# Performance work log

Hardware: AMD Instinct MI355X
Metric: run time of the kernel (lower is better)

Reference implementation:

```python
import jax, jax.numpy as jnp
import numpy as np

B, S, DIN, DIM = 4, 4096, 256, 256
GAMMA = 0.9865


def setup_inputs() -> dict:
    key = jax.random.key(0)
    ks = jax.random.split(key, 9)
    inp = {
        'xq': jax.random.normal(ks[0], (B, S, DIN), dtype=jnp.float32),
        'xk': jax.random.normal(ks[1], (B, S, DIN), dtype=jnp.float32),
        'xv': jax.random.normal(ks[2], (B, S, DIN), dtype=jnp.float32),
        'Wq': jax.random.normal(ks[3], (DIN, DIM), dtype=jnp.float32) * 0.05,
        'bq': jnp.zeros((DIM,), dtype=jnp.float32),
        'Wk': jax.random.normal(ks[4], (DIN, DIM), dtype=jnp.float32) * 0.05,
        'bk': jnp.zeros((DIM,), dtype=jnp.float32),
        'Wv': jax.random.normal(ks[5], (DIN, DIM), dtype=jnp.float32) * 0.05,
        'bv': jnp.zeros((DIM,), dtype=jnp.float32),
    }
    return inp


def _decay_matrix(s, gamma):
    # D[i, j] = gamma^(i-j) if i >= j else 0
    idx = jnp.arange(s)
    diff = idx[:, None] - idx[None, :]
    D = jnp.where(diff >= 0,
                  jnp.power(jnp.float32(gamma), diff.astype(jnp.float32)),
                  jnp.float32(0.0))
    return D


def reference(xq, xk, xv, Wq, bq, Wk, bk, Wv, bv):
    Q = xq @ Wq + bq  # [B,S,D]
    K = xk @ Wk + bk  # [B,S,D]
    V = xv @ Wv + bv  # [B,S,D]
    d = Q.shape[-1]
    # scores[b,i,j] = Q[b,i] . K[b,j] / sqrt(d)
    x = jnp.einsum('bid,bjd->bij', Q, K) / jnp.sqrt(jnp.float32(d))
    D = _decay_matrix(S, GAMMA)
    # Faithful to TF broadcasting: divides along the LAST axis (per-column by
    # sqrt of that index's row-sum): D[i,j] /= sqrt(sum_k D[j,k])
    D = D / jnp.sqrt(jnp.sum(D, axis=-1))
    x = x * D  # broadcast [B,S,S] * [S,S]
    # _norm_3 per batch element with TF broadcasting: x[b,i,j] /= max(|sum_k x[b,j,k]|, 1)
    denom = jnp.maximum(jnp.abs(jnp.sum(x, axis=-1)), 1.0)  # [B,S]
    x = x / denom[:, None, :]
    return x @ V  # [B,S,D]
```

## Files before the change

### kernel.cpp

```cpp
#include <hip/hip_runtime.h>
#include <math.h>

#define BB 4
#define SS 4096
#define DD 256
#define LL 256
#define NCH 16
#define GAMMA 0.9865f
#define LOG2G (-0.019609034f)
#define INV1MG 74.07407407f
#define SLAB 1032
#define SLABB 520

typedef __attribute__((ext_vector_type(8))) short short8;
typedef __attribute__((ext_vector_type(4))) float f32x4;
typedef unsigned short u16;
typedef unsigned int u32;

__device__ __forceinline__ u16 f2bf(float f) {
  union { float f; unsigned u; } v; v.f = f;
  unsigned r = v.u + 0x7FFFu + ((v.u >> 16) & 1u);
  return (u16)(r >> 16);
}
__device__ __forceinline__ float bf2f(u16 h) {
  union { unsigned u; float f; } v; v.u = ((unsigned)h) << 16; return v.f;
}

__device__ __forceinline__ void gll16(const u16* g, u16* l) {
  __builtin_amdgcn_global_load_lds(
      (const __attribute__((address_space(1))) u32*)g,
      (__attribute__((address_space(3))) u32*)l, 16, 0, 0);
}
__device__ __forceinline__ void stage8kp(const u16* g, u16* l, int lane) {
#pragma unroll
  for (int i = 0; i < 8; ++i)
    gll16(g + i * 512 + lane * 8, l + (i >> 1) * SLAB + (i & 1) * 512);
}

__device__ __forceinline__ void mfma_step_regB64(
    const u16* Ah, const u16* Al, const short8 bh[4], const short8 bl[4],
    int fm, int fq, f32x4 acc[4][4])
{
  const int ka = fq * SLABB;
  short8 ah[4], al[4];
#pragma unroll
  for (int i = 0; i < 4; ++i) {
    ah[i] = *(const short8*)&Ah[ka + (i * 16 + fm) * 8];
    al[i] = *(const short8*)&Al[ka + (i * 16 + fm) * 8];
  }
#pragma unroll
  for (int j = 0; j < 4; ++j)
#pragma unroll
    for (int i = 0; i < 4; ++i) {
      acc[i][j] = __builtin_amdgcn_mfma_f32_16x16x32_bf16(al[i], bh[j], acc[i][j], 0, 0, 0);
      acc[i][j] = __builtin_amdgcn_mfma_f32_16x16x32_bf16(ah[i], bl[j], acc[i][j], 0, 0, 0);
      acc[i][j] = __builtin_amdgcn_mfma_f32_16x16x32_bf16(ah[i], bh[j], acc[i][j], 0, 0, 0);
    }
}

__device__ __forceinline__ void mfma_step_regB_ab(
    const u16* Ah, const u16* Al, const short8 bh[2], const short8 bl[2],
    int wm0, int fm, int fq, f32x4 acc[4][2])
{
  const int ka = fq * SLAB;
  short8 ah[4], al[4];
#pragma unroll
  for (int i = 0; i < 4; ++i) {
    ah[i] = *(const short8*)&Ah[ka + (wm0 + i * 16 + fm) * 8];
    al[i] = *(const short8*)&Al[ka + (wm0 + i * 16 + fm) * 8];
  }
#pragma unroll
  for (int j = 0; j < 2; ++j)
#pragma unroll
    for (int i = 0; i < 4; ++i) {
      acc[i][j] = __builtin_amdgcn_mfma_f32_16x16x32_bf16(al[i], bh[j], acc[i][j], 0, 0, 0);
      acc[i][j] = __builtin_amdgcn_mfma_f32_16x16x32_bf16(ah[i], bl[j], acc[i][j], 0, 0, 0);
      acc[i][j] = __builtin_amdgcn_mfma_f32_16x16x32_bf16(ah[i], bh[j], acc[i][j], 0, 0, 0);
    }
}

__device__ __forceinline__ void loadB2(short8 bh[2], short8 bl[2],
    const u16* BhP, const u16* BlP, int ks, int wn0, int fm, int fq)
{
  const int base = ks * 4096 + fq * 1024;
#pragma unroll
  for (int j = 0; j < 2; ++j) {
    int o = base + (wn0 + j * 16 + fm) * 8;
    bh[j] = *(const short8*)&BhP[o];
    bl[j] = *(const short8*)&BlP[o];
  }
}

__device__ __forceinline__ void mfma_step_ab(
    const u16* Ah, const u16* Al, const u16* Bh, const u16* Bl,
    int wm0, int wn0, int fm, int fq, f32x4 acc[4][2])
{
  const int ka = fq * SLAB, kb = fq * SLABB;
  short8 ah[4], al[4];
#pragma unroll
  for (int i = 0; i < 4; ++i) {
    ah[i] = *(const short8*)&Ah[ka + (wm0 + i * 16 + fm) * 8];
    al[i] = *(const short8*)&Al[ka + (wm0 + i * 16 + fm) * 8];
  }
#pragma unroll
  for (int j = 0; j < 2; ++j) {
    short8 bh = *(const short8*)&Bh[kb + (wn0 + j * 16 + fm) * 8];
    short8 bl = *(const short8*)&Bl[kb + (wn0 + j * 16 + fm) * 8];
#pragma unroll
    for (int i = 0; i < 4; ++i) {
      acc[i][j] = __builtin_amdgcn_mfma_f32_16x16x32_bf16(al[i], bh, acc[i][j], 0, 0, 0);
      acc[i][j] = __builtin_amdgcn_mfma_f32_16x16x32_bf16(ah[i], bl, acc[i][j], 0, 0, 0);
      acc[i][j] = __builtin_amdgcn_mfma_f32_16x16x32_bf16(ah[i], bh, acc[i][j], 0, 0, 0);
    }
  }
}

__global__ __launch_bounds__(256) void init_pack_kernel(
    const float* __restrict__ Wq, const float* __restrict__ Wk, const float* __restrict__ Wv,
    u16* __restrict__ Wth, u16* __restrict__ Wtl,
    float* __restrict__ rsP, float* __restrict__ lVec)
{
  const int which = blockIdx.x;
  const int it = blockIdx.y;
  const int t = threadIdx.x;
  if (which == 0) {
    *(float4*)&rsP[(size_t)(it * 256 + t) * 4] = (float4){0.f, 0.f, 0.f, 0.f};
  } else if (which == 1) {
    *(float4*)&lVec[(size_t)(it * 256 + t) * 4] = (float4){0.f, 0.f, 0.f, 0.f};
  }
  const float* W = which == 0 ? Wq : (which == 1 ? Wk : Wv);
  for (int pn = 0; pn < 2; ++pn) {
    int pos = it * 256 + t;
    int k8 = pos >> 7, r = pos & 127;
    u16 hs[8], ls[8];
#pragma unroll
    for (int u = 0; u < 8; ++u) {
      float x = W[(size_t)(k8 * 8 + u) * DD + pn * 128 + r];
      u16 h = f2bf(x); hs[u] = h; ls[u] = f2bf(x - bf2f(h));
    }
    size_t o = ((size_t)((which * 2 + pn) * 32 + k8)) * 1024 + (size_t)r * 8;
    *(short8*)&Wth[o] = *(short8*)hs;
    *(short8*)&Wtl[o] = *(short8*)ls;
  }
}

__global__ __launch_bounds__(256, 3) void proj_kernel(
    const float* __restrict__ xq, const float* __restrict__ xk, const float* __restrict__ xv,
    const u16* __restrict__ Wth, const u16* __restrict__ Wtl,
    const float* __restrict__ bq, const float* __restrict__ bk_, const float* __restrict__ bv,
    u16* __restrict__ Qh, u16* __restrict__ Ql,
    u16* __restrict__ Kh, u16* __restrict__ Kl,
    u16* __restrict__ KTh, u16* __restrict__ KTl,
    u16* __restrict__ VTh, u16* __restrict__ VTl,
    float* __restrict__ lVec)
{
  const int which = blockIdx.z;
  const float* bias = which == 0 ? bq : (which == 1 ? bk_ : bv);
  const int m0 = blockIdx.x * 64;
  __shared__ u16 SM[16 * SLABB];
  __shared__ float rsc[64];
  __shared__ float wlut[64];
  __shared__ float kacc[64];
  float* fb = (float*)SM;
  const int tid = threadIdx.x, lane = tid & 63, wave = tid >> 6;
  const int wn0g = wave * 64;
  const int fm = lane & 15, fq = lane >> 4;
  if (which == 1 && tid < 64) {
    int sb = (m0 & (SS - 1)) + tid;
    rsc[tid] = rsqrtf((1.0f - exp2f((float)(sb + 1) * LOG2G)) * INV1MG);
    wlut[tid] = exp2f((float)(255 - ((m0 & (LL - 1)) + tid)) * LOG2G);
    kacc[tid] = 0.f;
  }
  const float* XP = (which == 0 ? xq : (which == 1 ? xk : xv)) + (size_t)m0 * DD;
  const int pnw = wn0g >> 7, wl = wn0g & 127;
  const u16* WhP = Wth + (size_t)((which * 2 + pnw) * 32) * 1024;
  const u16* WlP = Wtl + (size_t)((which * 2 + pnw) * 32) * 1024;
  const int arow = tid >> 2, ak8 = tid & 3;
  f32x4 acc[4][4];
#pragma unroll
  for (int i = 0; i < 4; ++i)
#pragma unroll
    for (int j = 0; j < 4; ++j) acc[i][j] = (f32x4){0.f, 0.f, 0.f, 0.f};
  float xs[8];
  short8 bh[4], bl[4];
  {
    const int base = fq * 1024;
#pragma unroll
    for (int j = 0; j < 4; ++j) {
      int o = base + (wl + j * 16 + fm) * 8;
      bh[j] = *(const short8*)&WhP[o];
      bl[j] = *(const short8*)&WlP[o];
    }
  }
  {
    const float* src = XP + (size_t)arow * DD + ak8 * 8;
    *(float4*)&xs[0] = *(const float4*)src;
    *(float4*)&xs[4] = *(const float4*)(src + 4);
    u16 hs[8], ls[8];
#pragma unroll
    for (int u = 0; u < 8; ++u) {
      u16 h = f2bf(xs[u]); hs[u] = h; ls[u] = f2bf(xs[u] - bf2f(h));
    }
    *(short8*)&SM[ak8 * SLABB + arow * 8] = *(short8*)hs;
    *(short8*)&SM[4 * SLABB + ak8 * SLABB + arow * 8] = *(short8*)ls;
  }
  int cur = 0;
  for (int ks = 0; ks < 8; ++ks) {
    __syncthreads();
    u16* Ac = SM + cur * 8 * SLABB;
    u16* An = SM + (cur ^ 1) * 8 * SLABB;
    if (ks < 7) {
      const float* src = XP + (size_t)arow * DD + (ks + 1) * 32 + ak8 * 8;
      *(float4*)&xs[0] = *(const float4*)src;
      *(float4*)&xs[4] = *(const float4*)(src + 4);
    }
    mfma_step_regB64(Ac, Ac + 4 * SLABB, bh, bl, fm, fq, acc);
    if (ks < 7) {
      const int base = (ks + 1) * 4096 + fq * 1024;
#pragma unroll
      for (int j = 0; j < 4; ++j) {
        int o = base + (wl + j * 16 + fm) * 8;
        bh[j] = *(const short8*)&WhP[o];
        bl[j] = *(const short8*)&WlP[o];
      }
      u16 hs[8], ls[8];
#pragma unroll
      for (int u = 0; u < 8; ++u) {
        u16 h = f2bf(xs[u]); hs[u] = h; ls[u] = f2bf(xs[u] - bf2f(h));
      }
      *(short8*)&An[ak8 * SLABB + arow * 8] = *(short8*)hs;
      *(short8*)&An[4 * SLABB + ak8 * SLABB + arow * 8] = *(short8*)ls;
    }
    cur ^= 1;
  }
  const int b = m0 >> 12, sbb = m0 & (SS - 1);
  for (int p = 0; p < 4; ++p) {
    __syncthreads();
    if (wn0g == p * 64) {
#pragma unroll
      for (int i = 0; i < 4; ++i)
#pragma unroll
        for (int j = 0; j < 4; ++j)
#pragma unroll
          for (int r = 0; r < 4; ++r)
            fb[(i * 16 + fq * 4 + r) * 65 + j * 16 + fm] = acc[i][j][r];
    }
    __syncthreads();
    if (which == 0) {
#pragma unroll
      for (int it = 0; it < 2; ++it) {
        int unit = it * 256 + tid;
        int k8l = unit >> 6, row = unit & 63;
        int gc0 = p * 64 + k8l * 8;
        u16 hs[8], ls[8];
#pragma unroll
        for (int u = 0; u < 8; ++u) {
          float v = (fb[row * 65 + k8l * 8 + u] + bias[gc0 + u]) * (1.f / 16.f);
          u16 h = f2bf(v); hs[u] = h; ls[u] = f2bf(v - bf2f(h));
        }
        size_t o = (size_t)(m0 >> 7) * 32768 + (size_t)(p * 8 + k8l) * 1024 +
                   (size_t)((m0 & 64) + row) * 8;
        *(short8*)&Qh[o] = *(short8*)hs;
        *(short8*)&Ql[o] = *(short8*)ls;
      }
    } else if (which == 1) {
#pragma unroll
      for (int it = 0; it < 2; ++it) {
        int unit = it * 256 + tid;
        int k8l = unit >> 6, row = unit & 63;
        int gc0 = p * 64 + k8l * 8;
        u16 hs[8], ls[8];
#pragma unroll
        for (int u = 0; u < 8; ++u) {
          float v = (fb[row * 65 + k8l * 8 + u] + bias[gc0 + u]) * rsc[row];
          u16 h = f2bf(v); hs[u] = h; ls[u] = f2bf(v - bf2f(h));
        }
        size_t o = (size_t)(m0 >> 7) * 32768 + (size_t)(p * 8 + k8l) * 1024 +
                   (size_t)((m0 & 64) + row) * 8;
        *(short8*)&Kh[o] = *(short8*)hs;
        *(short8*)&Kl[o] = *(short8*)ls;
      }
      float kpart = 0.f;
#pragma unroll
      for (int it = 0; it < 2; ++it) {
        int unit = it * 256 + tid;
        int dl = unit & 63, s8l = unit >> 6;
        int gcolg = p * 64 + dl;
        float bs = bias[gcolg];
        u16 hs[8], ls[8];
#pragma unroll
        for (int u = 0; u < 8; ++u) {
          int row = s8l * 8 + u;
          float v = (fb[row * 65 + dl] + bs) * rsc[row];
          kpart = fmaf(v, wlut[row], kpart);
          u16 h = f2bf(v); hs[u] = h; ls[u] = f2bf(v - bf2f(h));
        }
        int sb0 = sbb + s8l * 8;
        size_t o = ((size_t)(b * 2 + (gcolg >> 7)) * 512 + (sb0 >> 3)) * 1024 + (size_t)(gcolg & 127) * 8;
        *(short8*)&KTh[o] = *(short8*)hs;
        *(short8*)&KTl[o] = *(short8*)ls;
      }
      atomicAdd(&kacc[tid & 63], kpart);
      __syncthreads();
      if (tid < 64) {
        int c = sbb >> 8;
        atomicAdd(&lVec[(size_t)(b * NCH + c) * DD + p * 64 + tid], kacc[tid]);
        kacc[tid] = 0.f;
      }
    } else {
#pragma unroll
      for (int it = 0; it < 2; ++it) {
        int unit = it * 256 + tid;
        int dl = unit & 63, s8l = unit >> 6;
        int gcolg = p * 64 + dl;
        float bs = bias[gcolg];
        u16 hs[8], ls[8];
#pragma unroll
        for (int u = 0; u < 8; ++u) {
          float v = fb[(s8l * 8 + u) * 65 + dl] + bs;
          u16 h = f2bf(v); hs[u] = h; ls[u] = f2bf(v - bf2f(h));
        }
        int sb0 = sbb + s8l * 8;
        size_t o = ((size_t)(b * 2 + (gcolg >> 7)) * 512 + (sb0 >> 3)) * 1024 + (size_t)(gcolg & 127) * 8;
        *(short8*)&VTh[o] = *(short8*)hs;
        *(short8*)&VTl[o] = *(short8*)ls;
      }
    }
  }
}

__global__ __launch_bounds__(256, 4) void scores_kernel(
    const u16* __restrict__ Qh, const u16* __restrict__ Ql,
    const u16* __restrict__ Kh, const u16* __restrict__ Kl,
    const float* __restrict__ lVec, u16* __restrict__ Sgh, u16* __restrict__ Sgl,
    float* __restrict__ rsP)
{
  const int chunk = blockIdx.x, b = chunk >> 4, c = chunk & 15;
  const int y = blockIdx.y;
  const int m0 = (y < 2) ? 0 : 128;
  const int jn0 = (y < 2) ? y * 64 : (y - 2) * 64;
  __shared__ u16 SA[2 * 8 * SLAB];
  __shared__ float cv[256], lut[256], rowAcc[128], qd2[2][128];
  float* fb = (float*)SA;
  const int tid = threadIdx.x, lane = tid & 63, wave = tid >> 6;
  const int wm0 = (wave >> 1) * 64, wn0 = (wave & 1) * 32;
  const int fm = lane & 15, fq = lane >> 4;
  if (jn0 == 0) {
    const float gL = exp2f((float)LL * LOG2G);
    float s = 0.f;
    for (int cp = 0; cp < c; ++cp)
      s = fmaf(gL, s, lVec[(size_t)(b * NCH + cp) * DD + tid]);
    cv[tid] = s;
  }
  lut[tid] = exp2f((float)tid * LOG2G);
  if (tid < 128) rowAcc[tid] = 0.f;
  const int growA = b * SS + c * LL + m0;
  const int growB = b * SS + c * LL + jn0;
  const u16* QhP = Qh + (size_t)(growA >> 7) * 32768;
  const u16* QlP = Ql + (size_t)(growA >> 7) * 32768;
  const u16* KhP = Kh + (size_t)(growB >> 7) * 32768 + (size_t)(growB & 127) * 8;
  const u16* KlP = Kl + (size_t)(growB >> 7) * 32768 + (size_t)(growB & 127) * 8;
  f32x4 acc[4][2];
#pragma unroll
  for (int i = 0; i < 4; ++i)
#pragma unroll
    for (int j = 0; j < 2; ++j) acc[i][j] = (f32x4){0.f, 0.f, 0.f, 0.f};
  float qdreg = 0.f;
  const int qrow = tid & 127, qk8b = tid >> 7;
  short8 bh[2], bl[2];
  if (wave == 0) stage8kp(QhP, SA, lane);
  if (wave == 1) stage8kp(QlP, SA + 4 * SLAB, lane);
  loadB2(bh, bl, KhP, KlP, 0, wn0, fm, fq);
  int cur = 0;
  for (int ks = 0; ks < 8; ++ks) {
    __syncthreads();
    u16* Ac = cur ? SA + 8 * SLAB : SA;
    u16* An = cur ? SA : SA + 8 * SLAB;
    if (ks < 7) {
      if (wave == 0) stage8kp(QhP + (ks + 1) * 4096, An, lane);
      if (wave == 1) stage8kp(QlP + (ks + 1) * 4096, An + 4 * SLAB, lane);
    }
    mfma_step_regB_ab(Ac, Ac + 4 * SLAB, bh, bl, wm0, fm, fq, acc);
    if (ks < 7) loadB2(bh, bl, KhP, KlP, ks + 1, wn0, fm, fq);
    if (jn0 == 0) {
#pragma unroll
      for (int h2 = 0; h2 < 2; ++h2) {
        int k8l = qk8b + 2 * h2;
        const u16* ahp = &Ac[k8l * SLAB + qrow * 8];
        const u16* alp = &Ac[4 * SLAB + k8l * SLAB + qrow * 8];
#pragma unroll
        for (int u = 0; u < 8; ++u)
          qdreg = fmaf(bf2f(ahp[u]) + bf2f(alp[u]), cv[ks * 32 + k8l * 8 + u], qdreg);
      }
    }
    cur ^= 1;
  }
  qd2[qk8b][qrow] = qdreg;
  const int ps = chunk * 2 + (m0 >> 7);
  for (int rh = 0; rh < 2; ++rh) {
    __syncthreads();
    if (wm0 == rh * 64) {
#pragma unroll
      for (int i = 0; i < 4; ++i)
#pragma unroll
        for (int j = 0; j < 2; ++j)
#pragma unroll
          for (int r = 0; r < 4; ++r)
            fb[(i * 16 + fq * 4 + r) * 65 + wn0 + j * 16 + fm] = acc[i][j][r];
    }
    __syncthreads();
#pragma unroll
    for (int it = 0; it < 2; ++it) {
      int unit = it * 256 + tid;
      int k8l = unit >> 6, rowl = unit & 63;
      int il = m0 + rh * 64 + rowl;
      int jlb = jn0 + k8l * 8;
      float part = 0.f;
      u16 hs[8], ls[8];
#pragma unroll
      for (int u = 0; u < 8; ++u) {
        int jl = jlb + u;
        float v = (jl <= il) ? fb[rowl * 65 + k8l * 8 + u] * lut[il - jl] : 0.f;
        part += v;
        u16 h = f2bf(v); hs[u] = h; ls[u] = f2bf(v - bf2f(h));
      }
      atomicAdd(&rowAcc[rh * 64 + rowl], part);
      size_t o = (size_t)(ps * 32 + (jn0 >> 3) + k8l) * 1024 + (size_t)(rh * 64 + rowl) * 8;
      *(short8*)&Sgh[o] = *(short8*)hs;
      *(short8*)&Sgl[o] = *(short8*)ls;
    }
  }
  __syncthreads();
  if (tid < 128) {
    float rs = rowAcc[tid];
    if (jn0 == 0)
      rs += exp2f((float)(m0 + tid + 1) * LOG2G) * (qd2[0][tid] + qd2[1][tid]);
    atomicAdd(&rsP[(size_t)b * SS + c * LL + m0 + tid], rs);
  }
}

__global__ __launch_bounds__(256, 4) void lmat_kernel(
    const u16* __restrict__ VTh, const u16* __restrict__ VTl,
    const float* __restrict__ rsP,
    const u16* __restrict__ KTh, const u16* __restrict__ KTl,
    float* __restrict__ lMatT)
{
  const int chunk = blockIdx.x, b = chunk >> 4, c = chunk & 15;
  const int ty = blockIdx.y;
  const int m0 = (ty >> 2) * 128, n0 = (ty & 3) * 64;
  __shared__ u16 SA[2 * 8 * SLAB];
  __shared__ float swl[256];
  const int tid = threadIdx.x, lane = tid & 63, wave = tid >> 6;
  const int wm0 = (wave >> 1) * 64, wn0 = (wave & 1) * 32;
  const int fm = lane & 15, fq = lane >> 4;
  swl[tid] = exp2f((float)(255 - tid) * LOG2G) /
             fmaxf(fabsf(rsP[(size_t)b * SS + c * LL + tid]), 1.0f);
  const u16* AThP = VTh + ((size_t)(b * 2 + (m0 >> 7)) * 512 + c * 32) * 1024;
  const u16* ATlP = VTl + ((size_t)(b * 2 + (m0 >> 7)) * 512 + c * 32) * 1024;
  const u16* BhP = KTh + ((size_t)(b * 2 + (n0 >> 7)) * 512 + c * 32) * 1024 + (size_t)(n0 & 127) * 8;
  const u16* BlP = KTl + ((size_t)(b * 2 + (n0 >> 7)) * 512 + c * 32) * 1024 + (size_t)(n0 & 127) * 8;
  const int arow = tid >> 1;
  f32x4 acc[4][2];
#pragma unroll
  for (int i = 0; i < 4; ++i)
#pragma unroll
    for (int j = 0; j < 2; ++j) acc[i][j] = (f32x4){0.f, 0.f, 0.f, 0.f};
  short8 vh[2], vl[2];
  short8 bh[2], bl[2];
  loadB2(bh, bl, BhP, BlP, 0, wn0, fm, fq);
#pragma unroll
  for (int t = 0; t < 2; ++t) {
    int ak8 = (tid & 1) * 2 + t;
    int off = ak8 * 1024 + arow * 8;
    vh[t] = *(const short8*)&AThP[off];
    vl[t] = *(const short8*)&ATlP[off];
  }
  __syncthreads();
#pragma unroll
  for (int t = 0; t < 2; ++t) {
    int ak8 = (tid & 1) * 2 + t;
    u16 hs[8], ls[8];
#pragma unroll
    for (int u = 0; u < 8; ++u) {
      float v = (bf2f((u16)vh[t][u]) + bf2f((u16)vl[t][u])) * swl[ak8 * 8 + u];
      u16 h = f2bf(v); hs[u] = h; ls[u] = f2bf(v - bf2f(h));
    }
    *(short8*)&SA[ak8 * SLAB + arow * 8] = *(short8*)hs;
    *(short8*)&SA[4 * SLAB + ak8 * SLAB + arow * 8] = *(short8*)ls;
  }
  int cur = 0;
  for (int ks = 0; ks < 8; ++ks) {
    __syncthreads();
    u16* Ac = cur ? SA + 8 * SLAB : SA;
    u16* An = cur ? SA : SA + 8 * SLAB;
    if (ks < 7) {
#pragma unroll
      for (int t = 0; t < 2; ++t) {
        int ak8 = (tid & 1) * 2 + t;
        int off = ((ks + 1) * 4 + ak8) * 1024 + arow * 8;
        vh[t] = *(const short8*)&AThP[off];
        vl[t] = *(const short8*)&ATlP[off];
      }
    }
    mfma_step_regB_ab(Ac, Ac + 4 * SLAB, bh, bl, wm0, fm, fq, acc);
    if (ks < 7) {
      loadB2(bh, bl, BhP, BlP, ks + 1, wn0, fm, fq);
#pragma unroll
      for (int t = 0; t < 2; ++t) {
        int ak8 = (tid & 1) * 2 + t;
        u16 hs[8], ls[8];
#pragma unroll
        for (int u = 0; u < 8; ++u) {
          float v = (bf2f((u16)vh[t][u]) + bf2f((u16)vl[t][u])) *
                    swl[(ks + 1) * 32 + ak8 * 8 + u];
          u16 h = f2bf(v); hs[u] = h; ls[u] = f2bf(v - bf2f(h));
        }
        *(short8*)&An[ak8 * SLAB + arow * 8] = *(short8*)hs;
        *(short8*)&An[4 * SLAB + ak8 * SLAB + arow * 8] = *(short8*)ls;
      }
    }
    cur ^= 1;
  }
#pragma unroll
  for (int i = 0; i < 4; ++i)
#pragma unroll
    for (int j = 0; j < 2; ++j)
#pragma unroll
      for (int r = 0; r < 4; ++r) {
        int e = m0 + wm0 + i * 16 + fq * 4 + r;
        int d = n0 + wn0 + j * 16 + fm;
        lMatT[(size_t)chunk * 65536 + (size_t)e * 256 + d] = acc[i][j][r];
      }
}

__global__ __launch_bounds__(256) void combine_mat_kernel(
    const float* __restrict__ lMatT, u16* __restrict__ cMh, u16* __restrict__ cMl)
{
  const int t = blockIdx.x * 256 + threadIdx.x;
  const int b = t >> 13, rem = t & 8191;
  const int k8 = rem >> 8, e = rem & 255;
  const float gL = powf(GAMMA, (float)LL);
  float s[8] = {0.f, 0.f, 0.f, 0.f, 0.f, 0.f, 0.f, 0.f};
  for (int ch = 0; ch < 16; ++ch) {
    size_t ro = (size_t)(b * 16 + ch) * 65536 + (size_t)e * 256 + k8 * 8;
    float4 a0 = *(const float4*)&lMatT[ro];
    float4 a1 = *(const float4*)&lMatT[ro + 4];
    float vals[8] = {a0.x, a0.y, a0.z, a0.w, a1.x, a1.y, a1.z, a1.w};
    u16 hh[8], ll[8];
#pragma unroll
    for (int u = 0; u < 8; ++u) {
      u16 h = f2bf(s[u]); hh[u] = h; ll[u] = f2bf(s[u] - bf2f(h));
    }
    size_t wo = ((size_t)(((b * 16 + ch) * 2 + (e >> 7)) * 32 + k8)) * 1024 + (size_t)(e & 127) * 8;
    *(short8*)&cMh[wo] = *(short8*)hh;
    *(short8*)&cMl[wo] = *(short8*)ll;
#pragma unroll
    for (int u = 0; u < 8; ++u) s[u] = gL * s[u] + vals[u];
  }
}

__global__ __launch_bounds__(256, 3) void out_kernel(
    const u16* __restrict__ Qh, const u16* __restrict__ Ql,
    const u16* __restrict__ cMh, const u16* __restrict__ cMl,
    const u16* __restrict__ Sgh, const u16* __restrict__ Sgl,
    const u16* __restrict__ VTh, const u16* __restrict__ VTl,
    const float* __restrict__ rsP,
    float* __restrict__ out)
{
  const int chunk = blockIdx.x, b = chunk >> 4, c = chunk & 15;
  const int ty = blockIdx.y;
  const int m0 = (ty >> 2) * 128, n0 = (ty & 3) * 64;
  __shared__ u16 SA[2 * 8 * SLAB];
  __shared__ u16 SB[2 * 8 * SLABB];
  __shared__ float olut[128];
  __shared__ float sdn[256];
  const int tid = threadIdx.x, lane = tid & 63, wave = tid >> 6;
  const int wm0 = (wave >> 1) * 64, wn0 = (wave & 1) * 32;
  const int fm = lane & 15, fq = lane >> 4;
  if (tid < 128) olut[tid] = exp2f((float)(m0 + tid + 1) * LOG2G);
  sdn[tid] = 1.0f / fmaxf(fabsf(rsP[(size_t)b * SS + c * LL + tid]), 1.0f);
  f32x4 acc[4][2];
#pragma unroll
  for (int i = 0; i < 4; ++i)
#pragma unroll
    for (int j = 0; j < 2; ++j) acc[i][j] = (f32x4){0.f, 0.f, 0.f, 0.f};
  int cur = 0;
  {
    const u16* AhP = Qh + (size_t)(b * 32 + c * 2 + (m0 >> 7)) * 32768;
    const u16* AlP = Ql + (size_t)(b * 32 + c * 2 + (m0 >> 7)) * 32768;
    const u16* BhP = cMh + (size_t)(chunk * 2 + (n0 >> 7)) * 32768 + (size_t)(n0 & 127) * 8;
    const u16* BlP = cMl + (size_t)(chunk * 2 + (n0 >> 7)) * 32768 + (size_t)(n0 & 127) * 8;
    short8 bh[2], bl[2];
    if (wave == 0) stage8kp(AhP, SA, lane);
    if (wave == 1) stage8kp(AlP, SA + 4 * SLAB, lane);
    loadB2(bh, bl, BhP, BlP, 0, wn0, fm, fq);
    for (int ks = 0; ks < 8; ++ks) {
      __syncthreads();
      u16* Ac = cur ? SA + 8 * SLAB : SA;
      u16* An = cur ? SA : SA + 8 * SLAB;
      if (ks < 7) {
        if (wave == 0) stage8kp(AhP + (ks + 1) * 4096, An, lane);
        if (wave == 1) stage8kp(AlP + (ks + 1) * 4096, An + 4 * SLAB, lane);
      }
      mfma_step_regB_ab(Ac, Ac + 4 * SLAB, bh, bl, wm0, fm, fq, acc);
      if (ks < 7) loadB2(bh, bl, BhP, BlP, ks + 1, wn0, fm, fq);
      cur ^= 1;
    }
  }
  {
    const u16* AhP = Sgh + (size_t)(chunk * 2 + (m0 >> 7)) * 32768;
    const u16* AlP = Sgl + (size_t)(chunk * 2 + (m0 >> 7)) * 32768;
    const u16* BThP = VTh + ((size_t)(b * 2 + (n0 >> 7)) * 512 + c * 32) * 1024 + (size_t)(n0 & 127) * 8;
    const u16* BTlP = VTl + ((size_t)(b * 2 + (n0 >> 7)) * 512 + c * 32) * 1024 + (size_t)(n0 & 127) * 8;
    const int ber = tid >> 2, bk8 = tid & 3;
    const int nks = (m0 >> 5) + 4;
    short8 vh, vl;
    {
      u16* Ac = cur ? SA + 8 * SLAB : SA;
      u16* Bc = cur ? SB + 8 * SLABB : SB;
      if (wave == 0) stage8kp(AhP, Ac, lane);
      if (wave == 1) stage8kp(AlP, Ac + 4 * SLAB, lane);
      int off = bk8 * 1024 + ber * 8;
      vh = *(const short8*)&BThP[off];
      vl = *(const short8*)&BTlP[off];
#pragma unroll
      for (int i = 0; i < 4; ++i)
#pragma unroll
        for (int r = 0; r < 4; ++r) {
          int rl = wm0 + i * 16 + fq * 4 + r;
          float sc = olut[rl];
#pragma unroll
          for (int j = 0; j < 2; ++j) acc[i][j][r] *= sc;
        }
      u16 hs[8], ls[8];
#pragma unroll
      for (int u = 0; u < 8; ++u) {
        float v = (bf2f((u16)vh[u]) + bf2f((u16)vl[u])) * sdn[bk8 * 8 + u];
        u16 h = f2bf(v); hs[u] = h; ls[u] = f2bf(v - bf2f(h));
      }
      *(short8*)&Bc[bk8 * SLABB + ber * 8] = *(short8*)hs;
      *(short8*)&Bc[4 * SLABB + bk8 * SLABB + ber * 8] = *(short8*)ls;
    }
    for (int ks = 0; ks < nks; ++ks) {
      __syncthreads();
      u16* Ac = cur ? SA + 8 * SLAB : SA;
      u16* Bc = cur ? SB + 8 * SLABB : SB;
      u16* An = cur ? SA : SA + 8 * SLAB;
      u16* Bn = cur ? SB : SB + 8 * SLABB;
      if (ks + 1 < nks) {
        if (wave == 0) stage8kp(AhP + (ks + 1) * 4096, An, lane);
        if (wave == 1) stage8kp(AlP + (ks + 1) * 4096, An + 4 * SLAB, lane);
        int off = ((ks + 1) * 4 + bk8) * 1024 + ber * 8;
        vh = *(const short8*)&BThP[off];
        vl = *(const short8*)&BTlP[off];
      }
      mfma_step_ab(Ac, Ac + 4 * SLAB, Bc, Bc + 4 * SLABB, wm0, wn0, fm, fq, acc);
      if (ks + 1 < nks) {
        u16 hs[8], ls[8];
#pragma unroll
        for (int u = 0; u < 8; ++u) {
          float v = (bf2f((u16)vh[u]) + bf2f((u16)vl[u])) *
                    sdn[(ks + 1) * 32 + bk8 * 8 + u];
          u16 h = f2bf(v); hs[u] = h; ls[u] = f2bf(v - bf2f(h));
        }
        *(short8*)&Bn[bk8 * SLABB + ber * 8] = *(short8*)hs;
        *(short8*)&Bn[4 * SLABB + bk8 * SLABB + ber * 8] = *(short8*)ls;
      }
      cur ^= 1;
    }
  }
#pragma unroll
  for (int i = 0; i < 4; ++i)
#pragma unroll
    for (int j = 0; j < 2; ++j)
#pragma unroll
      for (int r = 0; r < 4; ++r) {
        int il = m0 + wm0 + i * 16 + fq * 4 + r;
        int e = n0 + wn0 + j * 16 + fm;
        out[(size_t)(b * SS + c * LL + il) * DD + e] = acc[i][j][r];
      }
}

extern "C" void kernel_launch(void* const* d_in, const int* in_sizes, int n_in,
                              void* d_out, int out_size, void* d_ws, size_t ws_size,
                              hipStream_t stream) {
  const float* xq = (const float*)d_in[0];
  const float* xk = (const float*)d_in[1];
  const float* xv = (const float*)d_in[2];
  const float* Wq = (const float*)d_in[3];
  const float* bq = (const float*)d_in[4];
  const float* Wk = (const float*)d_in[5];
  const float* bk = (const float*)d_in[6];
  const float* Wv = (const float*)d_in[7];
  const float* bv = (const float*)d_in[8];
  float* out = (float*)d_out;

  char* p = (char*)d_ws;
  const size_t H16 = (size_t)BB * SS * DD * 2;
  u16* Qh   = (u16*)(p + 0 * H16);  u16* Ql   = (u16*)(p + 1 * H16);
  u16* Kh   = (u16*)(p + 2 * H16);  u16* Kl   = (u16*)(p + 3 * H16);
  u16* KTh  = (u16*)(p + 4 * H16);  u16* KTl  = (u16*)(p + 5 * H16);
  u16* VTh  = (u16*)(p + 6 * H16);  u16* VTl  = (u16*)(p + 7 * H16);
  u16* Sgh  = (u16*)(p + 10 * H16); u16* Sgl  = (u16*)(p + 11 * H16);
  u16* cMh  = (u16*)(p + 12 * H16); u16* cMl  = (u16*)(p + 13 * H16);
  float* lMatT = (float*)(p + 14 * H16);
  u16* Wth = (u16*)(p + 18 * H16);
  u16* Wtl = (u16*)(p + 18 * H16 + 3 * DD * DD * 2);
  float* rsP  = (float*)(p + 18 * H16 + 6 * DD * DD * 2);
  float* lVec = rsP + (size_t)BB * SS;

  init_pack_kernel<<<dim3(3, 16), 256, 0, stream>>>(Wq, Wk, Wv, Wth, Wtl, rsP, lVec);
  proj_kernel<<<dim3(BB * SS / 64, 1, 3), 256, 0, stream>>>(
      xq, xk, xv, Wth, Wtl, bq, bk, bv, Qh, Ql, Kh, Kl, KTh, KTl, VTh, VTl, lVec);
  scores_kernel<<<dim3(BB * NCH, 6), 256, 0, stream>>>(
      Qh, Ql, Kh, Kl, lVec, Sgh, Sgl, rsP);
  lmat_kernel<<<dim3(BB * NCH, 8), 256, 0, stream>>>(VTh, VTl, rsP, KTh, KTl, lMatT);
  combine_mat_kernel<<<128, 256, 0, stream>>>(lMatT, cMh, cMl);
  out_kernel<<<dim3(BB * NCH, 8), 256, 0, stream>>>(
      Qh, Ql, cMh, cMl, Sgh, Sgl, VTh, VTl, rsP, out);
}
```

Before: 198.2 us.

## Shrink scores and lmat tiles to 64x64 for more blocks and finer causal skip

The scores kernel now uses 64x64 tiles over the lower-triangular block pairs within each chunk, giving 10 tiles instead of 6 with 128-row tiles. This skips more of the work above the diagonal, and the diagonal-tile fix-up is simplified to a single pass. The lmat kernel also moves to 64-row tiles, doubling its grid to 16 blocks per chunk. Both changes raise block count and occupancy at the cost of smaller per-wave MFMA tiles, less operand reuse, and more redundant K/B loads.

```diff
diff --git a/kernel.cpp b/kernel.cpp
--- a/kernel.cpp
+++ b/kernel.cpp
@@ -36,6 +36,11 @@
   for (int i = 0; i < 8; ++i)
     gll16(g + i * 512 + lane * 8, l + (i >> 1) * SLAB + (i & 1) * 512);
 }
+__device__ __forceinline__ void stageB64(const u16* g, u16* l, int lane) {
+#pragma unroll
+  for (int i = 0; i < 4; ++i)
+    gll16(g + i * 1024 + lane * 8, l + i * SLABB);
+}
 
 __device__ __forceinline__ void mfma_step_regB64(
     const u16* Ah, const u16* Al, const short8 bh[4], const short8 bl[4],
@@ -52,6 +57,27 @@
   for (int j = 0; j < 4; ++j)
 #pragma unroll
     for (int i = 0; i < 4; ++i) {
+      acc[i][j] = __builtin_amdgcn_mfma_f32_16x16x32_bf16(al[i], bh[j], acc[i][j], 0, 0, 0);
+      acc[i][j] = __builtin_amdgcn_mfma_f32_16x16x32_bf16(ah[i], bl[j], acc[i][j], 0, 0, 0);
+      acc[i][j] = __builtin_amdgcn_mfma_f32_16x16x32_bf16(ah[i], bh[j], acc[i][j], 0, 0, 0);
+    }
+}
+
+__device__ __forceinline__ void mfma_64_ab(
+    const u16* Ah, const u16* Al, const short8 bh[2], const short8 bl[2],
+    int wm0, int fm, int fq, f32x4 acc[2][2])
+{
+  const int ka = fq * SLABB;
+  short8 ah[2], al[2];
+#pragma unroll
+  for (int i = 0; i < 2; ++i) {
+    ah[i] = *(const short8*)&Ah[ka + (wm0 + i * 16 + fm) * 8];
+    al[i] = *(const short8*)&Al[ka + (wm0 + i * 16 + fm) * 8];
+  }
+#pragma unroll
+  for (int j = 0; j < 2; ++j)
+#pragma unroll
+    for (int i = 0; i < 2; ++i) {
       acc[i][j] = __builtin_amdgcn_mfma_f32_16x16x32_bf16(al[i], bh[j], acc[i][j], 0, 0, 0);
       acc[i][j] = __builtin_amdgcn_mfma_f32_16x16x32_bf16(ah[i], bl[j], acc[i][j], 0, 0, 0);
       acc[i][j] = __builtin_amdgcn_mfma_f32_16x16x32_bf16(ah[i], bh[j], acc[i][j], 0, 0, 0);
@@ -337,13 +363,14 @@
 {
   const int chunk = blockIdx.x, b = chunk >> 4, c = chunk & 15;
   const int y = blockIdx.y;
-  const int m0 = (y < 2) ? 0 : 128;
-  const int jn0 = (y < 2) ? y * 64 : (y - 2) * 64;
-  __shared__ u16 SA[2 * 8 * SLAB];
-  __shared__ float cv[256], lut[256], rowAcc[128], qd2[2][128];
+  const int mi = (y >= 6) ? 3 : (y >= 3) ? 2 : (y >= 1) ? 1 : 0;
+  const int ji = y - mi * (mi + 1) / 2;
+  const int m0 = mi * 64, jn0 = ji * 64;
+  __shared__ u16 SA[2 * 8 * SLABB];
+  __shared__ float cv[256], lut[256], rowAcc[64], qd4[4][64];
   float* fb = (float*)SA;
   const int tid = threadIdx.x, lane = tid & 63, wave = tid >> 6;
-  const int wm0 = (wave >> 1) * 64, wn0 = (wave & 1) * 32;
+  const int wm0 = (wave >> 1) * 32, wn0 = (wave & 1) * 32;
   const int fm = lane & 15, fq = lane >> 4;
   if (jn0 == 0) {
     const float gL = exp2f((float)LL * LOG2G);
@@ -353,88 +380,83 @@
     cv[tid] = s;
   }
   lut[tid] = exp2f((float)tid * LOG2G);
-  if (tid < 128) rowAcc[tid] = 0.f;
+  if (tid < 64) rowAcc[tid] = 0.f;
   const int growA = b * SS + c * LL + m0;
   const int growB = b * SS + c * LL + jn0;
-  const u16* QhP = Qh + (size_t)(growA >> 7) * 32768;
-  const u16* QlP = Ql + (size_t)(growA >> 7) * 32768;
+  const u16* QhP = Qh + (size_t)(growA >> 7) * 32768 + (size_t)(growA & 127) * 8;
+  const u16* QlP = Ql + (size_t)(growA >> 7) * 32768 + (size_t)(growA & 127) * 8;
   const u16* KhP = Kh + (size_t)(growB >> 7) * 32768 + (size_t)(growB & 127) * 8;
   const u16* KlP = Kl + (size_t)(growB >> 7) * 32768 + (size_t)(growB & 127) * 8;
-  f32x4 acc[4][2];
-#pragma unroll
-  for (int i = 0; i < 4; ++i)
+  f32x4 acc[2][2];
+#pragma unroll
+  for (int i = 0; i < 2; ++i)
 #pragma unroll
     for (int j = 0; j < 2; ++j) acc[i][j] = (f32x4){0.f, 0.f, 0.f, 0.f};
   float qdreg = 0.f;
-  const int qrow = tid & 127, qk8b = tid >> 7;
+  const int qrow = tid & 63, qk8b = tid >> 6;
   short8 bh[2], bl[2];
-  if (wave == 0) stage8kp(QhP, SA, lane);
-  if (wave == 1) stage8kp(QlP, SA + 4 * SLAB, lane);
+  if (wave == 0) stageB64(QhP, SA, lane);
+  if (wave == 1) stageB64(QlP, SA + 4 * SLABB, lane);
   loadB2(bh, bl, KhP, KlP, 0, wn0, fm, fq);
   int cur = 0;
   for (int ks = 0; ks < 8; ++ks) {
     __syncthreads();
-    u16* Ac = cur ? SA + 8 * SLAB : SA;
-    u16* An = cur ? SA : SA + 8 * SLAB;
+    u16* Ac = cur ? SA + 8 * SLABB : SA;
+    u16* An = cur ? SA : SA + 8 * SLABB;
     if (ks < 7) {
-      if (wave == 0) stage8kp(QhP + (ks + 1) * 4096, An, lane);
-      if (wave == 1) stage8kp(QlP + (ks + 1) * 4096, An + 4 * SLAB, lane);
-    }
-    mfma_step_regB_ab(Ac, Ac + 4 * SLAB, bh, bl, wm0, fm, fq, acc);
+      if (wave == 0) stageB64(QhP + (ks + 1) * 4096, An, lane);
+      if (wave == 1) stageB64(QlP + (ks + 1) * 4096, An + 4 * SLABB, lane);
+    }
+    mfma_64_ab(Ac, Ac + 4 * SLABB, bh, bl, wm0, fm, fq, acc);
     if (ks < 7) loadB2(bh, bl, KhP, KlP, ks + 1, wn0, fm, fq);
     if (jn0 == 0) {
-#pragma unroll
-      for (int h2 = 0; h2 < 2; ++h2) {
-        int k8l = qk8b + 2 * h2;
-        const u16* ahp = &Ac[k8l * SLAB + qrow * 8];
-        const u16* alp = &Ac[4 * SLAB + k8l * SLAB + qrow * 8];
-#pragma unroll
-        for (int u = 0; u < 8; ++u)
-          qdreg = fmaf(bf2f(ahp[u]) + bf2f(alp[u]), cv[ks * 32 + k8l * 8 + u], qdreg);
-      }
+      short8 hv = *(const short8*)&Ac[qk8b * SLABB + qrow * 8];
+      short8 lv = *(const short8*)&Ac[4 * SLABB + qk8b * SLABB + qrow * 8];
+#pragma unroll
+      for (int u = 0; u < 8; ++u)
+        qdreg = fmaf(bf2f((u16)hv[u]) + bf2f((u16)lv[u]),
+                     cv[ks * 32 + qk8b * 8 + u], qdreg);
     }
     cur ^= 1;
   }
-  qd2[qk8b][qrow] = qdreg;
+  qd4[qk8b][qrow] = qdreg;
   const int ps = chunk * 2 + (m0 >> 7);
-  for (int rh = 0; rh < 2; ++rh) {
-    __syncthreads();
-    if (wm0 == rh * 64) {
-#pragma unroll
-      for (int i = 0; i < 4; ++i)
-#pragma unroll
-        for (int j = 0; j < 2; ++j)
-#pragma unroll
-          for (int r = 0; r < 4; ++r)
-            fb[(i * 16 + fq * 4 + r) * 65 + wn0 + j * 16 + fm] = acc[i][j][r];
-    }
-    __syncthreads();
-#pragma unroll
-    for (int it = 0; it < 2; ++it) {
-      int unit = it * 256 + tid;
-      int k8l = unit >> 6, rowl = unit & 63;
-      int il = m0 + rh * 64 + rowl;
-      int jlb = jn0 + k8l * 8;
-      float part = 0.f;
-      u16 hs[8], ls[8];
-#pragma unroll
-      for (int u = 0; u < 8; ++u) {
-        int jl = jlb + u;
-        float v = (jl <= il) ? fb[rowl * 65 + k8l * 8 + u] * lut[il - jl] : 0.f;
-        part += v;
-        u16 h = f2bf(v); hs[u] = h; ls[u] = f2bf(v - bf2f(h));
-      }
-      atomicAdd(&rowAcc[rh * 64 + rowl], part);
-      size_t o = (size_t)(ps * 32 + (jn0 >> 3) + k8l) * 1024 + (size_t)(rh * 64 + rowl) * 8;
-      *(short8*)&Sgh[o] = *(short8*)hs;
-      *(short8*)&Sgl[o] = *(short8*)ls;
-    }
-  }
   __syncthreads();
-  if (tid < 128) {
+#pragma unroll
+  for (int i = 0; i < 2; ++i)
+#pragma unroll
+    for (int j = 0; j < 2; ++j)
+#pragma unroll
+      for (int r = 0; r < 4; ++r)
+        fb[(wm0 + i * 16 + fq * 4 + r) * 65 + wn0 + j * 16 + fm] = acc[i][j][r];
+  __syncthreads();
+#pragma unroll
+  for (int it = 0; it < 2; ++it) {
+    int unit = it * 256 + tid;
+    int k8l = unit >> 6, rowl = unit & 63;
+    int il = m0 + rowl;
+    int jlb = jn0 + k8l * 8;
+    float part = 0.f;
+    u16 hs[8], ls[8];
+#pragma unroll
+    for (int u = 0; u < 8; ++u) {
+      int jl = jlb + u;
+      float v = (jl <= il) ? fb[rowl * 65 + k8l * 8 + u] * lut[il - jl] : 0.f;
+      part += v;
+      u16 h = f2bf(v); hs[u] = h; ls[u] = f2bf(v - bf2f(h));
+    }
+    atomicAdd(&rowAcc[rowl], part);
+    size_t o = (size_t)(ps * 32 + (jn0 >> 3) + k8l) * 1024 +
+               (size_t)((m0 & 64) + rowl) * 8;
+    *(short8*)&Sgh[o] = *(short8*)hs;
+    *(short8*)&Sgl[o] = *(short8*)ls;
+  }
+  __syncthreads();
+  if (tid < 64) {
     float rs = rowAcc[tid];
     if (jn0 == 0)
-      rs += exp2f((float)(m0 + tid + 1) * LOG2G) * (qd2[0][tid] + qd2[1][tid]);
+      rs += exp2f((float)(m0 + tid + 1) * LOG2G) *
+            (qd4[0][tid] + qd4[1][tid] + qd4[2][tid] + qd4[3][tid]);
     atomicAdd(&rsP[(size_t)b * SS + c * LL + m0 + tid], rs);
   }
 }
@@ -447,82 +469,72 @@
 {
   const int chunk = blockIdx.x, b = chunk >> 4, c = chunk & 15;
   const int ty = blockIdx.y;
-  const int m0 = (ty >> 2) * 128, n0 = (ty & 3) * 64;
-  __shared__ u16 SA[2 * 8 * SLAB];
+  const int m0 = (ty >> 2) * 64, n0 = (ty & 3) * 64;
+  __shared__ u16 SA[2 * 8 * SLABB];
   __shared__ float swl[256];
   const int tid = threadIdx.x, lane = tid & 63, wave = tid >> 6;
-  const int wm0 = (wave >> 1) * 64, wn0 = (wave & 1) * 32;
+  const int wm0 = (wave >> 1) * 32, wn0 = (wave & 1) * 32;
   const int fm = lane & 15, fq = lane >> 4;
   swl[tid] = exp2f((float)(255 - tid) * LOG2G) /
              fmaxf(fabsf(rsP[(size_t)b * SS + c * LL + tid]), 1.0f);
-  const u16* AThP = VTh + ((size_t)(b * 2 + (m0 >> 7)) * 512 + c * 32) * 1024;
-  const u16* ATlP = VTl + ((size_t)(b * 2 + (m0 >> 7)) * 512 + c * 32) * 1024;
+  const u16* AThP = VTh + ((size_t)(b * 2 + (m0 >> 7)) * 512 + c * 32) * 1024 +
+                    (size_t)(m0 & 127) * 8;
+  const u16* ATlP = VTl + ((size_t)(b * 2 + (m0 >> 7)) * 512 + c * 32) * 1024 +
+                    (size_t)(m0 & 127) * 8;
   const u16* BhP = KTh + ((size_t)(b * 2 + (n0 >> 7)) * 512 + c * 32) * 1024 + (size_t)(n0 & 127) * 8;
   const u16* BlP = KTl + ((size_t)(b * 2 + (n0 >> 7)) * 512 + c * 32) * 1024 + (size_t)(n0 & 127) * 8;
-  const int arow = tid >> 1;
-  f32x4 acc[4][2];
-#pragma unroll
-  for (int i = 0; i < 4; ++i)
+  const int arow = tid >> 2, ak8 = tid & 3;
+  f32x4 acc[2][2];
+#pragma unroll
+  for (int i = 0; i < 2; ++i)
 #pragma unroll
     for (int j = 0; j < 2; ++j) acc[i][j] = (f32x4){0.f, 0.f, 0.f, 0.f};
-  short8 vh[2], vl[2];
+  short8 vh, vl;
   short8 bh[2], bl[2];
   loadB2(bh, bl, BhP, BlP, 0, wn0, fm, fq);
-#pragma unroll
-  for (int t = 0; t < 2; ++t) {
-    int ak8 = (tid & 1) * 2 + t;
+  {
     int off = ak8 * 1024 + arow * 8;
-    vh[t] = *(const short8*)&AThP[off];
-    vl[t] = *(const short8*)&ATlP[off];
+    vh = *(const short8*)&AThP[off];
+    vl = *(const short8*)&ATlP[off];
   }
   __syncthreads();
-#pragma unroll
-  for (int t = 0; t < 2; ++t) {
-    int ak8 = (tid & 1) * 2 + t;
+  {
     u16 hs[8], ls[8];
 #pragma unroll
     for (int u = 0; u < 8; ++u) {
-      float v = (bf2f((u16)vh[t][u]) + bf2f((u16)vl[t][u])) * swl[ak8 * 8 + u];
+      float v = (bf2f((u16)vh[u]) + bf2f((u16)vl[u])) * swl[ak8 * 8 + u];
       u16 h = f2bf(v); hs[u] = h; ls[u] = f2bf(v - bf2f(h));
     }
-    *(short8*)&SA[ak8 * SLAB + arow * 8] = *(short8*)hs;
-    *(short8*)&SA[4 * SLAB + ak8 * SLAB + arow * 8] = *(short8*)ls;
+    *(short8*)&SA[ak8 * SLABB + arow * 8] = *(short8*)hs;
+    *(short8*)&SA[4 * SLABB + ak8 * SLABB + arow * 8] = *(short8*)ls;
   }
   int cur = 0;
   for (int ks = 0; ks < 8; ++ks) {
     __syncthreads();
-    u16* Ac = cur ? SA + 8 * SLAB : SA;
-    u16* An = cur ? SA : SA + 8 * SLAB;
+    u16* Ac = cur ? SA + 8 * SLABB : SA;
+    u16* An = cur ? SA : SA + 8 * SLABB;
     if (ks < 7) {
-#pragma unroll
-      for (int t = 0; t < 2; ++t) {
-        int ak8 = (tid & 1) * 2 + t;
-        int off = ((ks + 1) * 4 + ak8) * 1024 + arow * 8;
-        vh[t] = *(const short8*)&AThP[off];
-        vl[t] = *(const short8*)&ATlP[off];
-      }
-    }
-    mfma_step_regB_ab(Ac, Ac + 4 * SLAB, bh, bl, wm0, fm, fq, acc);
+      int off = ((ks + 1) * 4 + ak8) * 1024 + arow * 8;
+      vh = *(const short8*)&AThP[off];
+      vl = *(const short8*)&ATlP[off];
+    }
+    mfma_64_ab(Ac, Ac + 4 * SLABB, bh, bl, wm0, fm, fq, acc);
     if (ks < 7) {
       loadB2(bh, bl, BhP, BlP, ks + 1, wn0, fm, fq);
-#pragma unroll
-      for (int t = 0; t < 2; ++t) {
-        int ak8 = (tid & 1) * 2 + t;
-        u16 hs[8], ls[8];
-#pragma unroll
-        for (int u = 0; u < 8; ++u) {
-          float v = (bf2f((u16)vh[t][u]) + bf2f((u16)vl[t][u])) *
-                    swl[(ks + 1) * 32 + ak8 * 8 + u];
-          u16 h = f2bf(v); hs[u] = h; ls[u] = f2bf(v - bf2f(h));
-        }
-        *(short8*)&An[ak8 * SLAB + arow * 8] = *(short8*)hs;
-        *(short8*)&An[4 * SLAB + ak8 * SLAB + arow * 8] = *(short8*)ls;
-      }
+      u16 hs[8], ls[8];
+#pragma unroll
+      for (int u = 0; u < 8; ++u) {
+        float v = (bf2f((u16)vh[u]) + bf2f((u16)vl[u])) *
+                  swl[(ks + 1) * 32 + ak8 * 8 + u];
+        u16 h = f2bf(v); hs[u] = h; ls[u] = f2bf(v - bf2f(h));
+      }
+      *(short8*)&An[ak8 * SLABB + arow * 8] = *(short8*)hs;
+      *(short8*)&An[4 * SLABB + ak8 * SLABB + arow * 8] = *(short8*)ls;
     }
     cur ^= 1;
   }
 #pragma unroll
-  for (int i = 0; i < 4; ++i)
+  for (int i = 0; i < 2; ++i)
 #pragma unroll
     for (int j = 0; j < 2; ++j)
 #pragma unroll
@@ -712,9 +724,9 @@
   init_pack_kernel<<<dim3(3, 16), 256, 0, stream>>>(Wq, Wk, Wv, Wth, Wtl, rsP, lVec);
   proj_kernel<<<dim3(BB * SS / 64, 1, 3), 256, 0, stream>>>(
       xq, xk, xv, Wth, Wtl, bq, bk, bv, Qh, Ql, Kh, Kl, KTh, KTl, VTh, VTl, lVec);
-  scores_kernel<<<dim3(BB * NCH, 6), 256, 0, stream>>>(
+  scores_kernel<<<dim3(BB * NCH, 10), 256, 0, stream>>>(
       Qh, Ql, Kh, Kl, lVec, Sgh, Sgl, rsP);
-  lmat_kernel<<<dim3(BB * NCH, 8), 256, 0, stream>>>(VTh, VTl, rsP, KTh, KTl, lMatT);
+  lmat_kernel<<<dim3(BB * NCH, 16), 256, 0, stream>>>(VTh, VTl, rsP, KTh, KTl, lMatT);
   combine_mat_kernel<<<128, 256, 0, stream>>>(lMatT, cMh, cMl);
   out_kernel<<<dim3(BB * NCH, 8), 256, 0, stream>>>(
       Qh, Ql, cMh, cMl, Sgh, Sgl, VTh, VTl, rsP, out);
```

Result: no change. 197.0 us (-0.6%).
